# Kernel optimization log

Measured on AMD Instinct MI355X. Metric: run time of the kernel, lower is better.

Reference implementation:

```python
import jax, jax.numpy as jnp
import numpy as np

STACK, N, I, D, K = 2, 32, 4096, 128, 16


def setup_inputs() -> dict:
    key = jax.random.key(0)
    k1, k2 = jax.random.split(key)
    feature_matrix_batch = jax.random.normal(k1, (STACK, N, I, D), dtype=jnp.float32)
    # cluster id in [0, K) per point, offset so point-cloud n uses segments [n*K, (n+1)*K)
    local = jax.random.randint(k2, (STACK, N, I), 0, K)
    offset = (jnp.arange(N) * K)[None, :, None]  # [1, N, 1]
    cluster_index = (local + offset).reshape(STACK, N * I).astype(jnp.int64)
    return {"feature_matrix_batch": feature_matrix_batch, "cluster_index": cluster_index}


def reference(feature_matrix_batch, cluster_index):
    # feature_matrix_batch: [S, N, I, D]; cluster_index: [S, N*I] in [0, N*K)
    S, n, i, d = feature_matrix_batch.shape

    def one(f, idx):
        flat = f.reshape(n * i, d)                       # [N*I, D]
        seg = jax.ops.segment_max(flat, idx, num_segments=n * K)  # [N*K, D]
        return seg.reshape(n, K, d)                       # [N, K, D]

    return jax.vmap(one)(feature_matrix_batch, cluster_index)  # [S, N, K, D]
```

## Files before the change

kernel.cpp:

```cpp
#include <hip/hip_runtime.h>
#include <math.h>

#define S_ 2
#define N_ 32
#define I_ 4096
#define D_ 128
#define K_ 16
#define C_ 16
#define P_ (I_ / C_)
#define THREADS 256
#define WAVES 4
#define KD (K_ * D_)

__global__ __launch_bounds__(THREADS) void maxpool_main(
    const float* __restrict__ F,
    const int*   __restrict__ IDX,
    float*       __restrict__ WS)
{
    __shared__ float acc[WAVES * KD];
    __shared__ int   kidx[P_];

    const int blk  = blockIdx.x;
    const int c    = blk % C_;
    const int sn   = blk / C_;
    const int base = c * P_;
    const int tid  = threadIdx.x;

    #pragma unroll
    for (int i = tid; i < WAVES * KD; i += THREADS) acc[i] = -INFINITY;
    kidx[tid] = IDX[sn * I_ + base + tid] & (K_ - 1);
    __syncthreads();

    const int w    = tid >> 6;
    const int lane = tid & 63;
    float* priv = acc + w * KD;
    const float2* src = (const float2*)(F + (size_t)(sn * I_ + base) * D_);

    #pragma unroll 4
    for (int it = 0; it < P_ / WAVES; ++it) {
        const int p = it * WAVES + w;
        const int k = kidx[p];
        const float2 v = src[(size_t)p * (D_ / 2) + lane];
        float2* a = (float2*)(priv + k * D_ + lane * 2);
        float2 o = *a;
        o.x = fmaxf(o.x, v.x);
        o.y = fmaxf(o.y, v.y);
        *a = o;
    }
    __syncthreads();

    float* dst = WS + (size_t)blk * KD;
    #pragma unroll
    for (int e = tid; e < KD; e += THREADS) {
        float m = fmaxf(fmaxf(acc[e],          acc[e + KD]),
                        fmaxf(acc[e + 2 * KD], acc[e + 3 * KD]));
        dst[e] = m;
    }
}

__global__ __launch_bounds__(256) void maxpool_combine(
    const float* __restrict__ WS,
    float*       __restrict__ OUT)
{
    const int i  = blockIdx.x * 256 + threadIdx.x;
    const int sn = i >> 11;
    const int e  = i & (KD - 1);
    const float* p = WS + ((size_t)sn * C_) * KD + e;
    float m = -INFINITY;
    #pragma unroll
    for (int c = 0; c < C_; ++c) m = fmaxf(m, p[(size_t)c * KD]);
    OUT[i] = m;
}

extern "C" void kernel_launch(void* const* d_in, const int* in_sizes, int n_in,
                              void* d_out, int out_size, void* d_ws, size_t ws_size,
                              hipStream_t stream) {
    const float* F   = (const float*)d_in[0];
    const int*   IDX = (const int*)d_in[1];
    float*       WS  = (float*)d_ws;
    float*       OUT = (float*)d_out;

    maxpool_main<<<S_ * N_ * C_, THREADS, 0, stream>>>(F, IDX, WS);
    maxpool_combine<<<(S_ * N_ * KD) / 256, 256, 0, stream>>>(WS, OUT);
}
```

Before: 195.5 us.

## Fuse segment-max into one kernel with a block per cluster, compacted gather

Replaces the two-kernel scheme (per-chunk LDS histogram of maxima plus a combine pass) with one kernel that gives each block a single (cloud, cluster) pair. Each block first scans the cloud's indices and uses ballot and popcount to build a compacted list of matching points. It then gathers those feature rows with eight loads in flight per wave, keeping the running max in registers. This removes the LDS read-modify-write traffic, the workspace round trip and the second launch. The cost is that every block rereads all indices of its cloud, and the fixed 1024-entry point list assumes no cluster grows beyond that size.

```diff
diff --git a/kernel.cpp b/kernel.cpp
--- a/kernel.cpp
+++ b/kernel.cpp
@@ -6,70 +6,81 @@
 #define I_ 4096
 #define D_ 128
 #define K_ 16
-#define C_ 16
-#define P_ (I_ / C_)
 #define THREADS 256
 #define WAVES 4
-#define KD (K_ * D_)
+#define GROUP 8
+#define MAXPTS 1024
 
-__global__ __launch_bounds__(THREADS) void maxpool_main(
+__global__ __launch_bounds__(THREADS) void maxpool_fused(
     const float* __restrict__ F,
     const int*   __restrict__ IDX,
-    float*       __restrict__ WS)
+    float*       __restrict__ OUT)
 {
-    __shared__ float acc[WAVES * KD];
-    __shared__ int   kidx[P_];
+    __shared__ int    plist[MAXPTS];
+    __shared__ int    cnt;
+    __shared__ float2 red[WAVES][64];
 
     const int blk  = blockIdx.x;
-    const int c    = blk % C_;
-    const int sn   = blk / C_;
-    const int base = c * P_;
+    const int sn   = blk >> 4;
+    const int k    = blk & (K_ - 1);
     const int tid  = threadIdx.x;
+    const int w    = tid >> 6;
+    const int lane = tid & 63;
 
-    #pragma unroll
-    for (int i = tid; i < WAVES * KD; i += THREADS) acc[i] = -INFINITY;
-    kidx[tid] = IDX[sn * I_ + base + tid] & (K_ - 1);
+    if (tid == 0) cnt = 0;
     __syncthreads();
 
-    const int w    = tid >> 6;
-    const int lane = tid & 63;
-    float* priv = acc + w * KD;
-    const float2* src = (const float2*)(F + (size_t)(sn * I_ + base) * D_);
-
-    #pragma unroll 4
-    for (int it = 0; it < P_ / WAVES; ++it) {
-        const int p = it * WAVES + w;
-        const int k = kidx[p];
-        const float2 v = src[(size_t)p * (D_ / 2) + lane];
-        float2* a = (float2*)(priv + k * D_ + lane * 2);
-        float2 o = *a;
-        o.x = fmaxf(o.x, v.x);
-        o.y = fmaxf(o.y, v.y);
-        *a = o;
+    const int* idxs = IDX + sn * I_;
+    for (int r = 0; r < I_ / THREADS; ++r) {
+        const int pos = r * THREADS + tid;
+        const bool m  = (idxs[pos] & (K_ - 1)) == k;
+        const unsigned long long bal = __ballot(m);
+        int base = 0;
+        if (lane == 0) base = atomicAdd(&cnt, __popcll(bal));
+        base = __shfl(base, 0);
+        if (m) {
+            const int off = __popcll(bal & ((1ull << lane) - 1ull));
+            plist[base + off] = pos;
+        }
     }
     __syncthreads();
+    const int nm = cnt;
 
-    float* dst = WS + (size_t)blk * KD;
-    #pragma unroll
-    for (int e = tid; e < KD; e += THREADS) {
-        float m = fmaxf(fmaxf(acc[e],          acc[e + KD]),
-                        fmaxf(acc[e + 2 * KD], acc[e + 3 * KD]));
-        dst[e] = m;
+    const float2* src = (const float2*)(F + (size_t)sn * I_ * D_);
+    float2 acc = make_float2(-INFINITY, -INFINITY);
+
+    int j = w;
+    while (j + (GROUP - 1) * WAVES < nm) {
+        int    pp[GROUP];
+        float2 v[GROUP];
+        #pragma unroll
+        for (int u = 0; u < GROUP; ++u) pp[u] = plist[j + u * WAVES];
+        #pragma unroll
+        for (int u = 0; u < GROUP; ++u)
+            v[u] = src[(size_t)pp[u] * (D_ / 2) + lane];
+        #pragma unroll
+        for (int u = 0; u < GROUP; ++u) {
+            acc.x = fmaxf(acc.x, v[u].x);
+            acc.y = fmaxf(acc.y, v[u].y);
+        }
+        j += GROUP * WAVES;
     }
-}
+    for (; j < nm; j += WAVES) {
+        const float2 v = src[(size_t)plist[j] * (D_ / 2) + lane];
+        acc.x = fmaxf(acc.x, v.x);
+        acc.y = fmaxf(acc.y, v.y);
+    }
 
-__global__ __launch_bounds__(256) void maxpool_combine(
-    const float* __restrict__ WS,
-    float*       __restrict__ OUT)
-{
-    const int i  = blockIdx.x * 256 + threadIdx.x;
-    const int sn = i >> 11;
-    const int e  = i & (KD - 1);
-    const float* p = WS + ((size_t)sn * C_) * KD + e;
-    float m = -INFINITY;
-    #pragma unroll
-    for (int c = 0; c < C_; ++c) m = fmaxf(m, p[(size_t)c * KD]);
-    OUT[i] = m;
+    red[w][lane] = acc;
+    __syncthreads();
+    if (tid < 64) {
+        const float2 a = red[0][tid], b = red[1][tid];
+        const float2 c = red[2][tid], d = red[3][tid];
+        float2 m;
+        m.x = fmaxf(fmaxf(a.x, b.x), fmaxf(c.x, d.x));
+        m.y = fmaxf(fmaxf(a.y, b.y), fmaxf(c.y, d.y));
+        ((float2*)(OUT + (size_t)blk * D_))[tid] = m;
+    }
 }
 
 extern "C" void kernel_launch(void* const* d_in, const int* in_sizes, int n_in,
@@ -77,9 +88,8 @@
                               hipStream_t stream) {
     const float* F   = (const float*)d_in[0];
     const int*   IDX = (const int*)d_in[1];
-    float*       WS  = (float*)d_ws;
     float*       OUT = (float*)d_out;
+    (void)d_ws; (void)ws_size;
 
-    maxpool_main<<<S_ * N_ * C_, THREADS, 0, stream>>>(F, IDX, WS);
-    maxpool_combine<<<(S_ * N_ * KD) / 256, 256, 0, stream>>>(WS, OUT);
+    maxpool_fused<<<S_ * N_ * K_, THREADS, 0, stream>>>(F, IDX, OUT);
 }
```

Result: no change. 198.7 us (+1.6%).
